# Kernel tuning notes

Hardware: AMD Instinct MI355X
Metric: run time of the kernel (lower is better)

Reference implementation:

```python
import jax, jax.numpy as jnp
import numpy as np

B, S, C, H = 2, 2048, 1024, 16
D = C // H  # head dim = 64
NEG = -1.0e12


def setup_inputs() -> dict:
    key = jax.random.key(0)
    kq, kk, kv, kw = jax.random.split(key, 4)
    q = jax.random.normal(kq, (B, S, C), dtype=jnp.float32)
    k = jax.random.normal(kk, (B, S, C), dtype=jnp.float32)
    v = jax.random.normal(kv, (B, S, C), dtype=jnp.float32)
    attention_mask = jnp.ones((B, 1, 1, S), dtype=jnp.bool_)
    W_proj = jax.random.normal(kw, (C, C), dtype=jnp.float32) * (1.0 / np.sqrt(C))
    return {"q": q, "k": k, "v": v, "attention_mask": attention_mask, "W_proj": W_proj}


def reference(q, k, v, attention_mask, W_proj):
    # split heads: [B,S,C] -> [B,S,H,D]
    qh = q.reshape(B, S, H, D) * (D ** -0.5)
    kh = k.reshape(B, S, H, D)
    vh = v.reshape(B, S, H, D)
    bias = (1.0 - attention_mask.astype(jnp.float32)) * NEG  # [B,1,1,S]
    scores = jnp.einsum('bqhc,bkhc->bhqk', qh, kh) + bias    # [B,H,S,S]
    weights = jax.nn.softmax(scores, axis=-1)
    out = jnp.einsum('bhqk,bkhc->bqhc', weights, vh)         # [B,S,H,D]
    out = out.reshape(B, S, C)
    return out @ W_proj.T  # torch Linear: y = x W^T
```

## Files before the change

kernel.cpp:

```cpp
#include <hip/hip_runtime.h>
#include <hip/hip_bf16.h>

#define BB 2
#define SS 2048
#define CCH 1024
#define HH 16
#define DD 64
#define QSCALE 0.18033688011112042f

typedef __bf16 bf16x8 __attribute__((ext_vector_type(8)));
typedef float f32x4 __attribute__((ext_vector_type(4)));

static __device__ __forceinline__ f32x4 mfma16(bf16x8 a, bf16x8 b, f32x4 c) {
    return __builtin_amdgcn_mfma_f32_16x16x32_bf16(a, b, c, 0, 0, 0);
}

static __device__ __forceinline__ unsigned short f2bf(float f) {
    __hip_bfloat16 h = __float2bfloat16(f);
    return __builtin_bit_cast(unsigned short, h);
}

static __device__ __forceinline__ unsigned int pk(float a, float b) {
    return (unsigned int)f2bf(a) | ((unsigned int)f2bf(b) << 16);
}

static __device__ __forceinline__ unsigned int cvtpk(float lo, float hi) {
    unsigned int r;
    asm("v_cvt_pk_bf16_f32 %0, %1, %2" : "=v"(r) : "v"(lo), "v"(hi));
    return r;
}

static __device__ __forceinline__ bf16x8 ldsfrag(const unsigned short* p) {
    return __builtin_bit_cast(bf16x8, *reinterpret_cast<const uint4*>(p));
}

__launch_bounds__(256)
__global__ void prep_qkv(const float* __restrict__ q, const float* __restrict__ k,
                         const float* __restrict__ v,
                         unsigned short* __restrict__ Qb,
                         unsigned short* __restrict__ Kb,
                         unsigned short* __restrict__ VTb) {
    __shared__ __align__(16) unsigned short LT[DD * 72];
    const int bx = blockIdx.x;
    const int st = bx & 31, h = (bx >> 5) & 15, b = bx >> 9;
    const int t = threadIdx.x;
    const int srow = t >> 2, part = t & 3;
    const int s = st * 64 + srow;

    const size_t gbase = (size_t)(b * SS + s) * CCH + h * DD + part * 16;
    const float4* qg = reinterpret_cast<const float4*>(q + gbase);
    const float4* kg = reinterpret_cast<const float4*>(k + gbase);
    const float4* vg = reinterpret_cast<const float4*>(v + gbase);
    float4 qv[4], kv[4], vv[4];
#pragma unroll
    for (int i = 0; i < 4; i++) { qv[i] = qg[i]; kv[i] = kg[i]; vv[i] = vg[i]; }

    const size_t obase = (size_t)((b * HH + h) * SS + s) * DD + part * 16;
    uint4 qo0, qo1, ko0, ko1;
    qo0.x = pk(qv[0].x * QSCALE, qv[0].y * QSCALE); qo0.y = pk(qv[0].z * QSCALE, qv[0].w * QSCALE);
    qo0.z = pk(qv[1].x * QSCALE, qv[1].y * QSCALE); qo0.w = pk(qv[1].z * QSCALE, qv[1].w * QSCALE);
    qo1.x = pk(qv[2].x * QSCALE, qv[2].y * QSCALE); qo1.y = pk(qv[2].z * QSCALE, qv[2].w * QSCALE);
    qo1.z = pk(qv[3].x * QSCALE, qv[3].y * QSCALE); qo1.w = pk(qv[3].z * QSCALE, qv[3].w * QSCALE);
    ko0.x = pk(kv[0].x, kv[0].y); ko0.y = pk(kv[0].z, kv[0].w);
    ko0.z = pk(kv[1].x, kv[1].y); ko0.w = pk(kv[1].z, kv[1].w);
    ko1.x = pk(kv[2].x, kv[2].y); ko1.y = pk(kv[2].z, kv[2].w);
    ko1.z = pk(kv[3].x, kv[3].y); ko1.w = pk(kv[3].z, kv[3].w);
    reinterpret_cast<uint4*>(Qb + obase)[0] = qo0;
    reinterpret_cast<uint4*>(Qb + obase)[1] = qo1;
    reinterpret_cast<uint4*>(Kb + obase)[0] = ko0;
    reinterpret_cast<uint4*>(Kb + obase)[1] = ko1;

    const float vf[16] = {vv[0].x, vv[0].y, vv[0].z, vv[0].w,
                          vv[1].x, vv[1].y, vv[1].z, vv[1].w,
                          vv[2].x, vv[2].y, vv[2].z, vv[2].w,
                          vv[3].x, vv[3].y, vv[3].z, vv[3].w};
#pragma unroll
    for (int i = 0; i < 16; i++) {
        const int d = part * 16 + i;
        LT[d * 72 + srow] = f2bf(vf[i]);
    }
    __syncthreads();
    const int d = t >> 2, p2 = t & 3;
    const uint4 a0 = reinterpret_cast<const uint4*>(&LT[d * 72 + p2 * 16])[0];
    const uint4 a1 = reinterpret_cast<const uint4*>(&LT[d * 72 + p2 * 16])[1];
    const size_t vbase = (size_t)((b * HH + h) * DD + d) * SS + st * 64 + p2 * 16;
    reinterpret_cast<uint4*>(VTb + vbase)[0] = a0;
    reinterpret_cast<uint4*>(VTb + vbase)[1] = a1;
}

__launch_bounds__(256)
__global__ void conv_w(const float* __restrict__ W, unsigned short* __restrict__ Wb) {
    const size_t idx = ((size_t)blockIdx.x * 256 + threadIdx.x) * 4;
    const float4 wv = *reinterpret_cast<const float4*>(W + idx);
    uint2 o;
    o.x = pk(wv.x, wv.y);
    o.y = pk(wv.z, wv.w);
    *reinterpret_cast<uint2*>(Wb + idx) = o;
}

__launch_bounds__(256, 4)
__global__ void flash(const unsigned short* __restrict__ Qb,
                      const unsigned short* __restrict__ Kb,
                      const unsigned short* __restrict__ VTb,
                      unsigned short* __restrict__ X) {
    __shared__ __align__(16) unsigned short LK[64 * 72];
    __shared__ __align__(16) unsigned short LV[64 * 72];
    __shared__ __align__(16) unsigned int LP[4][16 * 36];

    const int bx = (blockIdx.x & 7) * 128 + (blockIdx.x >> 3);
    const int qt = bx & 31, h = (bx >> 5) & 15, b = bx >> 9;
    const int t = threadIdx.x;
    const int w = t >> 6, lane = t & 63, quad = lane >> 4, r15 = lane & 15;

    const size_t rowQK = (size_t)(b * HH + h) * SS;
    const size_t rowV = (size_t)(b * HH + h) * DD;
    const int q0 = qt * 64 + w * 16;

    bf16x8 qf[2];
#pragma unroll
    for (int kc = 0; kc < 2; kc++) {
        const uint4 u = *reinterpret_cast<const uint4*>(
            Qb + (rowQK + q0 + r15) * DD + kc * 32 + quad * 8);
        qf[kc] = __builtin_bit_cast(bf16x8, u);
    }

    const f32x4 zv = {0.f, 0.f, 0.f, 0.f};
    f32x4 of[4];
#pragma unroll
    for (int nb = 0; nb < 4; nb++) of[nb] = zv;
    float rs = 0.f;

    const int srow = t >> 2, sch = (t & 3) * 16;
    const unsigned short* kg = Kb + (rowQK + srow) * DD + sch;
    const unsigned short* vg = VTb + (rowV + srow) * SS + sch;
    unsigned short* lk = &LK[srow * 72 + sch];
    unsigned short* lv = &LV[srow * 72 + sch];

    unsigned int* lpw = &LP[w][r15 * 36];

    uint4 kr0 = *reinterpret_cast<const uint4*>(kg);
    uint4 kr1 = *reinterpret_cast<const uint4*>(kg + 8);
    uint4 vr0 = *reinterpret_cast<const uint4*>(vg);
    uint4 vr1 = *reinterpret_cast<const uint4*>(vg + 8);

    for (int kt = 0; kt < 32; kt++) {
        __syncthreads();
        *reinterpret_cast<uint4*>(lk) = kr0;
        *reinterpret_cast<uint4*>(lk + 8) = kr1;
        *reinterpret_cast<uint4*>(lv) = vr0;
        *reinterpret_cast<uint4*>(lv + 8) = vr1;
        __syncthreads();
        if (kt < 31) {
            const size_t ko = (size_t)(kt + 1) * 64 * DD;
            kr0 = *reinterpret_cast<const uint4*>(kg + ko);
            kr1 = *reinterpret_cast<const uint4*>(kg + ko + 8);
            vr0 = *reinterpret_cast<const uint4*>(vg + (kt + 1) * 64);
            vr1 = *reinterpret_cast<const uint4*>(vg + (kt + 1) * 64 + 8);
        }

        f32x4 sc[4];
#pragma unroll
        for (int kb = 0; kb < 4; kb++) sc[kb] = zv;
#pragma unroll
        for (int kb = 0; kb < 4; kb++) {
            const bf16x8 bk0 = ldsfrag(&LK[(kb * 16 + r15) * 72 + quad * 8]);
            const bf16x8 bk1 = ldsfrag(&LK[(kb * 16 + r15) * 72 + 32 + quad * 8]);
            sc[kb] = mfma16(bk0, qf[0], sc[kb]);
            sc[kb] = mfma16(bk1, qf[1], sc[kb]);
        }

#pragma unroll
        for (int kb = 0; kb < 4; kb++) {
            const float p0 = exp2f(sc[kb][0]);
            const float p1 = exp2f(sc[kb][1]);
            const float p2 = exp2f(sc[kb][2]);
            const float p3 = exp2f(sc[kb][3]);
            rs += (p0 + p1) + (p2 + p3);
            uint2 d;
            d.x = cvtpk(p0, p1);
            d.y = cvtpk(p2, p3);
            *reinterpret_cast<uint2*>(lpw + 8 * kb + 2 * quad) = d;
        }

        __asm__ volatile("s_waitcnt lgkmcnt(0)" ::: "memory");

#pragma unroll
        for (int kc = 0; kc < 2; kc++) {
            const uint4 pu = *reinterpret_cast<const uint4*>(lpw + 16 * kc + 4 * quad);
            const bf16x8 pa = __builtin_bit_cast(bf16x8, pu);
#pragma unroll
            for (int nb = 0; nb < 4; nb++) {
                const bf16x8 bv = ldsfrag(&LV[(nb * 16 + r15) * 72 + kc * 32 + quad * 8]);
                of[nb] = mfma16(pa, bv, of[nb]);
            }
        }
    }

    rs += __shfl_xor(rs, 16);
    rs += __shfl_xor(rs, 32);
#pragma unroll
    for (int r = 0; r < 4; r++) {
        const float linv = 1.f / __shfl(rs, quad * 4 + r);
        const size_t s = (size_t)b * SS + q0 + quad * 4 + r;
#pragma unroll
        for (int nb = 0; nb < 4; nb++)
            X[s * CCH + h * DD + nb * 16 + r15] = f2bf(of[nb][r] * linv);
    }
}

__launch_bounds__(256)
__global__ void proj(const unsigned short* __restrict__ X,
                     const unsigned short* __restrict__ Wb,
                     float* __restrict__ Y) {
    __shared__ __align__(16) unsigned short LX[128 * 72];
    __shared__ __align__(16) unsigned short LW[64 * 72];
    const int bx = blockIdx.x;
    const int mt = bx >> 4, nt = bx & 15;
    const int m0 = mt * 128, n0 = nt * 64;
    const int t = threadIdx.x;
    const int w = t >> 6, lane = t & 63, quad = lane >> 4, r15 = lane & 15;
    const int mw = (w & 1) * 64, nw = (w >> 1) * 32;
    const int rowX = t >> 1, halfX = (t & 1) * 32;
    const int rowW = t >> 2, qW = (t & 3) * 16;

    const f32x4 zv = {0.f, 0.f, 0.f, 0.f};
    f32x4 acc[4][2];
#pragma unroll
    for (int am = 0; am < 4; am++)
#pragma unroll
        for (int bn = 0; bn < 2; bn++) acc[am][bn] = zv;

    for (int kt = 0; kt < 16; kt++) {
        __syncthreads();
        {
            const uint4* sx = reinterpret_cast<const uint4*>(
                X + (size_t)(m0 + rowX) * CCH + kt * 64 + halfX);
            uint4* dx = reinterpret_cast<uint4*>(&LX[rowX * 72 + halfX]);
#pragma unroll
            for (int i = 0; i < 4; i++) dx[i] = sx[i];
            const uint4* sw = reinterpret_cast<const uint4*>(
                Wb + (size_t)(n0 + rowW) * CCH + kt * 64 + qW);
            uint4* dw = reinterpret_cast<uint4*>(&LW[rowW * 72 + qW]);
            dw[0] = sw[0]; dw[1] = sw[1];
        }
        __syncthreads();

#pragma unroll
        for (int kc = 0; kc < 2; kc++) {
            bf16x8 af[4], bw[2];
#pragma unroll
            for (int i = 0; i < 4; i++)
                af[i] = ldsfrag(&LX[(mw + i * 16 + r15) * 72 + kc * 32 + quad * 8]);
#pragma unroll
            for (int i = 0; i < 2; i++)
                bw[i] = ldsfrag(&LW[(nw + i * 16 + r15) * 72 + kc * 32 + quad * 8]);
#pragma unroll
            for (int am = 0; am < 4; am++)
#pragma unroll
                for (int bn = 0; bn < 2; bn++)
                    acc[am][bn] = mfma16(af[am], bw[bn], acc[am][bn]);
        }
    }

#pragma unroll
    for (int am = 0; am < 4; am++)
#pragma unroll
        for (int bn = 0; bn < 2; bn++)
#pragma unroll
            for (int r = 0; r < 4; r++) {
                const int m = m0 + mw + am * 16 + quad * 4 + r;
                const int n = n0 + nw + bn * 16 + r15;
                Y[(size_t)m * CCH + n] = acc[am][bn][r];
            }
}

extern "C" void kernel_launch(void* const* d_in, const int* in_sizes, int n_in,
                              void* d_out, int out_size, void* d_ws, size_t ws_size,
                              hipStream_t stream) {
    (void)in_sizes; (void)n_in; (void)out_size; (void)ws_size;
    const float* q = (const float*)d_in[0];
    const float* k = (const float*)d_in[1];
    const float* v = (const float*)d_in[2];
    const float* W = (const float*)d_in[4];
    float* Y = (float*)d_out;

    const size_t NHSD = (size_t)BB * HH * SS * DD;
    unsigned short* Qb = (unsigned short*)d_ws;
    unsigned short* Kb = Qb + NHSD;
    unsigned short* VTb = Kb + NHSD;
    unsigned short* X = VTb + NHSD;
    unsigned short* Wb = X + (size_t)BB * SS * CCH;

    prep_qkv<<<dim3(BB * HH * (SS / 64)), dim3(256), 0, stream>>>(q, k, v, Qb, Kb, VTb);
    conv_w<<<dim3((CCH * CCH) / 1024), dim3(256), 0, stream>>>(W, Wb);
    flash<<<dim3(BB * HH * (SS / 64)), dim3(256), 0, stream>>>(Qb, Kb, VTb, X);
    proj<<<dim3((BB * SS / 128) * (CCH / 64)), dim3(256), 0, stream>>>(X, Wb, Y);
}
```

Before: 185.6 us.

## Restructure flash kernel with 32x32 MFMA, split-KV waves, and double-buffered swizzled LDS

Switches the flash attention kernel from 16x16x32 to 32x32x16 bf16 MFMA tiles. Each wave now handles 32 query rows and half of the key range, and the two halves are reduced through shared memory at the end. K/V tiles are double-buffered in XOR-swizzled LDS with one barrier per iteration. P is kept in registers via permlane32 swaps instead of a round trip through LDS, and s_setprio is raised around the MFMA groups. The intent is to cut LDS traffic, bank conflicts and barrier count. In exchange it adds a cross-wave reduction epilogue and higher register pressure from the 16-wide accumulators.

```diff
diff --git a/kernel.cpp b/kernel.cpp
--- a/kernel.cpp
+++ b/kernel.cpp
@@ -10,9 +10,13 @@
 
 typedef __bf16 bf16x8 __attribute__((ext_vector_type(8)));
 typedef float f32x4 __attribute__((ext_vector_type(4)));
+typedef float f32x16 __attribute__((ext_vector_type(16)));
 
 static __device__ __forceinline__ f32x4 mfma16(bf16x8 a, bf16x8 b, f32x4 c) {
     return __builtin_amdgcn_mfma_f32_16x16x32_bf16(a, b, c, 0, 0, 0);
+}
+static __device__ __forceinline__ f32x16 mfma32(bf16x8 a, bf16x8 b, f32x16 c) {
+    return __builtin_amdgcn_mfma_f32_32x32x16_bf16(a, b, c, 0, 0, 0);
 }
 
 static __device__ __forceinline__ unsigned short f2bf(float f) {
@@ -103,108 +107,154 @@
                       const unsigned short* __restrict__ Kb,
                       const unsigned short* __restrict__ VTb,
                       unsigned short* __restrict__ X) {
-    __shared__ __align__(16) unsigned short LK[64 * 72];
-    __shared__ __align__(16) unsigned short LV[64 * 72];
-    __shared__ __align__(16) unsigned int LP[4][16 * 36];
+    __shared__ __align__(16) unsigned short SMEM[16384];
 
     const int bx = (blockIdx.x & 7) * 128 + (blockIdx.x >> 3);
     const int qt = bx & 31, h = (bx >> 5) & 15, b = bx >> 9;
     const int t = threadIdx.x;
-    const int w = t >> 6, lane = t & 63, quad = lane >> 4, r15 = lane & 15;
+    const int w = t >> 6, lane = t & 63;
+    const int c31 = lane & 31, hh = lane >> 5;
+    const int qw = w & 1, kw = w >> 1;
 
     const size_t rowQK = (size_t)(b * HH + h) * SS;
     const size_t rowV = (size_t)(b * HH + h) * DD;
-    const int q0 = qt * 64 + w * 16;
-
-    bf16x8 qf[2];
-#pragma unroll
-    for (int kc = 0; kc < 2; kc++) {
-        const uint4 u = *reinterpret_cast<const uint4*>(
-            Qb + (rowQK + q0 + r15) * DD + kc * 32 + quad * 8);
-        qf[kc] = __builtin_bit_cast(bf16x8, u);
-    }
-
-    const f32x4 zv = {0.f, 0.f, 0.f, 0.f};
-    f32x4 of[4];
-#pragma unroll
-    for (int nb = 0; nb < 4; nb++) of[nb] = zv;
+    const int q0 = qt * 64 + qw * 32;
+
+    const unsigned short* gsrc;
+    unsigned short* lwr;
+    size_t gphase, ginstr;
+    if ((w & 1) == 0) {
+        const int row = lane >> 3, blk = lane & 7;
+        gsrc = Kb + (rowQK + (size_t)kw * 1024 + row) * 64 + blk * 8;
+        lwr = SMEM + kw * 4096 + row * 64 + ((blk ^ row) << 3);
+        gphase = 32 * 64; ginstr = 8 * 64;
+    } else {
+        const int row = lane >> 2, blk = lane & 3;
+        gsrc = VTb + (rowV + row) * SS + (size_t)kw * 1024 + blk * 8;
+        lwr = SMEM + 8192 + kw * 4096 + row * 32 + ((blk ^ ((row >> 1) & 3)) << 3);
+        gphase = 32; ginstr = 16 * SS;
+    }
+
+    bf16x8 qf0, qf1, qf2, qf3;
+    {
+        const unsigned short* qp = Qb + (rowQK + q0 + c31) * DD + hh * 8;
+        qf0 = ldsfrag(qp);
+        qf1 = ldsfrag(qp + 16);
+        qf2 = ldsfrag(qp + 32);
+        qf3 = ldsfrag(qp + 48);
+    }
+
+    const int krx = c31 & 7;
+    const int kfo0 = c31 * 64 + (((0 + hh) ^ krx) << 3);
+    const int kfo1 = c31 * 64 + (((2 + hh) ^ krx) << 3);
+    const int kfo2 = c31 * 64 + (((4 + hh) ^ krx) << 3);
+    const int kfo3 = c31 * 64 + (((6 + hh) ^ krx) << 3);
+    const int vx = (c31 >> 1) & 3;
+    const int vfo00 = (c31) * 32 + (((0 + hh) ^ vx) << 3);
+    const int vfo01 = (c31) * 32 + (((2 + hh) ^ vx) << 3);
+    const int vfo10 = (32 + c31) * 32 + (((0 + hh) ^ vx) << 3);
+    const int vfo11 = (32 + c31) * 32 + (((2 + hh) ^ vx) << 3);
+
+    f32x16 of0, of1;
+#pragma unroll
+    for (int r = 0; r < 16; r++) { of0[r] = 0.f; of1[r] = 0.f; }
     float rs = 0.f;
 
-    const int srow = t >> 2, sch = (t & 3) * 16;
-    const unsigned short* kg = Kb + (rowQK + srow) * DD + sch;
-    const unsigned short* vg = VTb + (rowV + srow) * SS + sch;
-    unsigned short* lk = &LK[srow * 72 + sch];
-    unsigned short* lv = &LV[srow * 72 + sch];
-
-    unsigned int* lpw = &LP[w][r15 * 36];
-
-    uint4 kr0 = *reinterpret_cast<const uint4*>(kg);
-    uint4 kr1 = *reinterpret_cast<const uint4*>(kg + 8);
-    uint4 vr0 = *reinterpret_cast<const uint4*>(vg);
-    uint4 vr1 = *reinterpret_cast<const uint4*>(vg + 8);
-
-    for (int kt = 0; kt < 32; kt++) {
+    uint4 sreg0, sreg1, sreg2, sreg3;
+    sreg0 = *reinterpret_cast<const uint4*>(gsrc);
+    sreg1 = *reinterpret_cast<const uint4*>(gsrc + ginstr);
+    sreg2 = *reinterpret_cast<const uint4*>(gsrc + 2 * ginstr);
+    sreg3 = *reinterpret_cast<const uint4*>(gsrc + 3 * ginstr);
+    *reinterpret_cast<uint4*>(lwr) = sreg0;
+    *reinterpret_cast<uint4*>(lwr + 512) = sreg1;
+    *reinterpret_cast<uint4*>(lwr + 1024) = sreg2;
+    *reinterpret_cast<uint4*>(lwr + 1536) = sreg3;
+    __syncthreads();
+
+    for (int j = 0; j < 32; j++) {
+        const int buf = j & 1;
+        if (j < 31) {
+            const unsigned short* gp = gsrc + (size_t)(j + 1) * gphase;
+            sreg0 = *reinterpret_cast<const uint4*>(gp);
+            sreg1 = *reinterpret_cast<const uint4*>(gp + ginstr);
+            sreg2 = *reinterpret_cast<const uint4*>(gp + 2 * ginstr);
+            sreg3 = *reinterpret_cast<const uint4*>(gp + 3 * ginstr);
+        }
+        const unsigned short* KB = SMEM + kw * 4096 + buf * 2048;
+        const unsigned short* VB = SMEM + 8192 + kw * 4096 + buf * 2048;
+
+        f32x16 sc;
+#pragma unroll
+        for (int r = 0; r < 16; r++) sc[r] = 0.f;
+        __builtin_amdgcn_s_setprio(1);
+        sc = mfma32(ldsfrag(KB + kfo0), qf0, sc);
+        sc = mfma32(ldsfrag(KB + kfo1), qf1, sc);
+        sc = mfma32(ldsfrag(KB + kfo2), qf2, sc);
+        sc = mfma32(ldsfrag(KB + kfo3), qf3, sc);
+        __builtin_amdgcn_s_setprio(0);
+
+        const float p0 = exp2f(sc[0]),  p1 = exp2f(sc[1]),  p2 = exp2f(sc[2]),  p3 = exp2f(sc[3]);
+        const float p4 = exp2f(sc[4]),  p5 = exp2f(sc[5]),  p6 = exp2f(sc[6]),  p7 = exp2f(sc[7]);
+        const float p8 = exp2f(sc[8]),  p9 = exp2f(sc[9]),  pa = exp2f(sc[10]), pb = exp2f(sc[11]);
+        const float pc = exp2f(sc[12]), pd = exp2f(sc[13]), pe = exp2f(sc[14]), pf = exp2f(sc[15]);
+        rs += ((p0 + p1) + (p2 + p3)) + ((p4 + p5) + (p6 + p7))
+            + ((p8 + p9) + (pa + pb)) + ((pc + pd) + (pe + pf));
+        unsigned int A = cvtpk(p0, p1), Bd = cvtpk(p2, p3);
+        unsigned int C = cvtpk(p4, p5), Dd = cvtpk(p6, p7);
+        unsigned int E = cvtpk(p8, p9), F = cvtpk(pa, pb);
+        unsigned int G = cvtpk(pc, pd), Hd = cvtpk(pe, pf);
+        asm("v_permlane32_swap_b32 %0, %1" : "+v"(A), "+v"(C));
+        asm("v_permlane32_swap_b32 %0, %1" : "+v"(Bd), "+v"(Dd));
+        asm("v_permlane32_swap_b32 %0, %1" : "+v"(E), "+v"(G));
+        asm("v_permlane32_swap_b32 %0, %1" : "+v"(F), "+v"(Hd));
+        const uint4 pu0 = {A, Bd, C, Dd};
+        const uint4 pu1 = {E, F, G, Hd};
+        const bf16x8 pa0 = __builtin_bit_cast(bf16x8, pu0);
+        const bf16x8 pa1 = __builtin_bit_cast(bf16x8, pu1);
+
+        __builtin_amdgcn_s_setprio(1);
+        of0 = mfma32(pa0, ldsfrag(VB + vfo00), of0);
+        of0 = mfma32(pa1, ldsfrag(VB + vfo01), of0);
+        of1 = mfma32(pa0, ldsfrag(VB + vfo10), of1);
+        of1 = mfma32(pa1, ldsfrag(VB + vfo11), of1);
+        __builtin_amdgcn_s_setprio(0);
+
+        if (j < 31) {
+            unsigned short* lp = lwr + (buf ^ 1) * 2048;
+            *reinterpret_cast<uint4*>(lp) = sreg0;
+            *reinterpret_cast<uint4*>(lp + 512) = sreg1;
+            *reinterpret_cast<uint4*>(lp + 1024) = sreg2;
+            *reinterpret_cast<uint4*>(lp + 1536) = sreg3;
+        }
         __syncthreads();
-        *reinterpret_cast<uint4*>(lk) = kr0;
-        *reinterpret_cast<uint4*>(lk + 8) = kr1;
-        *reinterpret_cast<uint4*>(lv) = vr0;
-        *reinterpret_cast<uint4*>(lv + 8) = vr1;
-        __syncthreads();
-        if (kt < 31) {
-            const size_t ko = (size_t)(kt + 1) * 64 * DD;
-            kr0 = *reinterpret_cast<const uint4*>(kg + ko);
-            kr1 = *reinterpret_cast<const uint4*>(kg + ko + 8);
-            vr0 = *reinterpret_cast<const uint4*>(vg + (kt + 1) * 64);
-            vr1 = *reinterpret_cast<const uint4*>(vg + (kt + 1) * 64 + 8);
-        }
-
-        f32x4 sc[4];
-#pragma unroll
-        for (int kb = 0; kb < 4; kb++) sc[kb] = zv;
-#pragma unroll
-        for (int kb = 0; kb < 4; kb++) {
-            const bf16x8 bk0 = ldsfrag(&LK[(kb * 16 + r15) * 72 + quad * 8]);
-            const bf16x8 bk1 = ldsfrag(&LK[(kb * 16 + r15) * 72 + 32 + quad * 8]);
-            sc[kb] = mfma16(bk0, qf[0], sc[kb]);
-            sc[kb] = mfma16(bk1, qf[1], sc[kb]);
-        }
-
-#pragma unroll
-        for (int kb = 0; kb < 4; kb++) {
-            const float p0 = exp2f(sc[kb][0]);
-            const float p1 = exp2f(sc[kb][1]);
-            const float p2 = exp2f(sc[kb][2]);
-            const float p3 = exp2f(sc[kb][3]);
-            rs += (p0 + p1) + (p2 + p3);
-            uint2 d;
-            d.x = cvtpk(p0, p1);
-            d.y = cvtpk(p2, p3);
-            *reinterpret_cast<uint2*>(lpw + 8 * kb + 2 * quad) = d;
-        }
-
-        __asm__ volatile("s_waitcnt lgkmcnt(0)" ::: "memory");
-
-#pragma unroll
-        for (int kc = 0; kc < 2; kc++) {
-            const uint4 pu = *reinterpret_cast<const uint4*>(lpw + 16 * kc + 4 * quad);
-            const bf16x8 pa = __builtin_bit_cast(bf16x8, pu);
-#pragma unroll
-            for (int nb = 0; nb < 4; nb++) {
-                const bf16x8 bv = ldsfrag(&LV[(nb * 16 + r15) * 72 + kc * 32 + quad * 8]);
-                of[nb] = mfma16(pa, bv, of[nb]);
-            }
-        }
-    }
-
-    rs += __shfl_xor(rs, 16);
+    }
+
     rs += __shfl_xor(rs, 32);
-#pragma unroll
-    for (int r = 0; r < 4; r++) {
-        const float linv = 1.f / __shfl(rs, quad * 4 + r);
-        const size_t s = (size_t)b * SS + q0 + quad * 4 + r;
-#pragma unroll
-        for (int nb = 0; nb < 4; nb++)
-            X[s * CCH + h * DD + nb * 16 + r15] = f2bf(of[nb][r] * linv);
+    float* FO = (float*)SMEM;
+    float* FOr = FO + 4096;
+    if (kw == 1) {
+#pragma unroll
+        for (int r = 0; r < 16; r++) FO[((qw * 2 + 0) * 16 + r) * 64 + lane] = of0[r];
+#pragma unroll
+        for (int r = 0; r < 16; r++) FO[((qw * 2 + 1) * 16 + r) * 64 + lane] = of1[r];
+        if (lane < 32) FOr[qw * 32 + lane] = rs;
+    }
+    __syncthreads();
+    if (kw == 0) {
+#pragma unroll
+        for (int r = 0; r < 16; r++) of0[r] += FO[((qw * 2 + 0) * 16 + r) * 64 + lane];
+#pragma unroll
+        for (int r = 0; r < 16; r++) of1[r] += FO[((qw * 2 + 1) * 16 + r) * 64 + lane];
+        rs += FOr[qw * 32 + c31];
+        const float linv = 1.f / rs;
+#pragma unroll
+        for (int r = 0; r < 16; r++) {
+            const int qr = (r & 3) + 8 * (r >> 2) + 4 * hh;
+            const float lv = __shfl(linv, qr);
+            const size_t s = (size_t)b * SS + q0 + qr;
+            X[s * CCH + h * DD + c31] = f2bf(of0[r] * lv);
+            X[s * CCH + h * DD + 32 + c31] = f2bf(of1[r] * lv);
+        }
     }
 }
 
```

Result: faster. 179.3 us (-3.4%).
